# Kernel optimization log

Measured on AMD Instinct MI355X. Metric: run time of the kernel, lower is better.

Reference implementation:

```python
import jax, jax.numpy as jnp
import numpy as np

NUM_HEADS = 12

def setup_inputs() -> dict:
    key = jax.random.key(0)
    k1, k2, k3 = jax.random.split(key, 3)
    B, N, D = 16, 1024, 768
    x = jax.random.normal(k1, (B, N, D), dtype=jnp.float32)
    w_qkv = jax.random.normal(k2, (D, 3 * D), dtype=jnp.float32) * (D ** -0.5)
    b_qkv = jnp.zeros((3 * D,), dtype=jnp.float32)
    w_proj = jax.random.normal(k3, (D, D), dtype=jnp.float32) * (D ** -0.5)
    b_proj = jnp.zeros((D,), dtype=jnp.float32)
    return {"x": x, "w_qkv": w_qkv, "b_qkv": b_qkv, "w_proj": w_proj, "b_proj": b_proj}

def reference(x, w_qkv, b_qkv, w_proj, b_proj):
    B, N, D = x.shape
    H = NUM_HEADS
    Hd = D // H
    scale = Hd ** -0.5
    qkv = x @ w_qkv + b_qkv                       # (B, N, 3D)
    qkv = qkv.reshape(B, N, 3, H, Hd)
    q, k, v = qkv[:, :, 0], qkv[:, :, 1], qkv[:, :, 2]  # (B, N, H, Hd)
    attn = jnp.einsum('bnhd,bmhd->bhnm', q, k) * scale  # (B, H, N, N)
    attn = jax.nn.softmax(attn, axis=-1)
    out = jnp.einsum('bhnm,bmhd->bnhd', attn, v).reshape(B, N, D)
    return out @ w_proj + b_proj
```

## Files before the change

kernel.cpp:

```cpp
#include <hip/hip_runtime.h>


typedef _Float16 half8 __attribute__((ext_vector_type(8)));
typedef _Float16 half4 __attribute__((ext_vector_type(4)));
typedef __fp16   fp16x2 __attribute__((ext_vector_type(2)));
typedef float    f32x4  __attribute__((ext_vector_type(4)));
typedef float    f32x16 __attribute__((ext_vector_type(16)));
typedef unsigned int u32x4 __attribute__((ext_vector_type(4)));

#define DI __device__ __forceinline__

constexpr int   BATCH  = 16;
constexpr int   SEQ    = 1024;
constexpr int   DM     = 768;
constexpr int   NH     = 12;
constexpr int   HD     = 64;
constexpr float SCALE  = 0.125f;
constexpr float LOG2E  = 1.4426950408889634f;

DI void async16(const _Float16* g, _Float16* l) {
  __builtin_amdgcn_global_load_lds(
      (const __attribute__((address_space(1))) void*)g,
      (__attribute__((address_space(3))) void*)l, 16, 0, 0);
}

DI void copy16(_Float16* dst, const _Float16* src) {
  *(u32x4*)dst = *(const u32x4*)src;
}

DI int pack_rtz(float a, float b) {
  union { fp16x2 h; int i; } u;
  u.h = __builtin_amdgcn_cvt_pkrtz(a, b);
  return u.i;
}

__global__ void cvt_x_kernel(const float* __restrict__ x,
                             _Float16* __restrict__ xh, int n4) {
  int i = blockIdx.x * 256 + threadIdx.x;
  if (i >= n4) return;
  float4 v = ((const float4*)x)[i];
  half4 h;
  h[0] = (_Float16)v.x; h[1] = (_Float16)v.y;
  h[2] = (_Float16)v.z; h[3] = (_Float16)v.w;
  *(half4*)(xh + (size_t)i * 4) = h;
}

__global__ void cvt_wt_kernel(const float* __restrict__ w,
                              _Float16* __restrict__ wt, int K, int N) {
  __shared__ float tile[32][33];
  int kb = blockIdx.x * 32, nb = blockIdx.y * 32;
  int tx = threadIdx.x & 31, ty = threadIdx.x >> 5;
#pragma unroll
  for (int i = 0; i < 32; i += 8)
    tile[ty + i][tx] = w[(size_t)(kb + ty + i) * N + nb + tx];
  __syncthreads();
#pragma unroll
  for (int i = 0; i < 32; i += 8)
    wt[(size_t)(nb + ty + i) * K + kb + tx] = (_Float16)tile[tx][ty + i];
}

__launch_bounds__(256)
__global__ void gemm_qkv_kernel(const _Float16* __restrict__ A,
                                const _Float16* __restrict__ Bt,
                                const float* __restrict__ bias,
                                _Float16* __restrict__ Qo,
                                _Float16* __restrict__ Ko,
                                _Float16* __restrict__ VTo) {
  __shared__ _Float16 As[128 * 32];
  __shared__ _Float16 Bs[128 * 32];
  __shared__ _Float16 Cs[128 * 136];
  const int tid  = threadIdx.x;
  const int ct   = blockIdx.x;
  const int m0   = blockIdx.y * 128;
  const int n0   = ct * 128;
  const int w    = tid >> 6, lane = tid & 63;
  const int quad = lane >> 4, l15 = lane & 15;
  const int wr   = w >> 1, wc = w & 1;

  f32x4 acc[4][4] = {};

  const int e  = tid * 8;
  const int rA = e >> 5;
  const int kA = e & 31;
  const _Float16* ga = A  + (size_t)(m0 + rA) * 768 + kA;
  const _Float16* gb = Bt + (size_t)(n0 + rA) * 768 + kA;

  for (int kt = 0; kt < 24; ++kt) {
    __syncthreads();
    const int k0 = kt * 32;
    async16(ga + k0,            &As[e]);
    async16(ga + k0 + 64 * 768, &As[e + 2048]);
    async16(gb + k0,            &Bs[e]);
    async16(gb + k0 + 64 * 768, &Bs[e + 2048]);
    __syncthreads();

    half8 af[4], bf[4];
#pragma unroll
    for (int mi = 0; mi < 4; mi++)
      af[mi] = *(const half8*)&As[(wr * 64 + mi * 16 + l15) * 32 + quad * 8];
#pragma unroll
    for (int ni = 0; ni < 4; ni++)
      bf[ni] = *(const half8*)&Bs[(wc * 64 + ni * 16 + l15) * 32 + quad * 8];
#pragma unroll
    for (int mi = 0; mi < 4; mi++)
#pragma unroll
      for (int ni = 0; ni < 4; ni++)
        acc[mi][ni] = __builtin_amdgcn_mfma_f32_16x16x32_f16(
            af[mi], bf[ni], acc[mi][ni], 0, 0, 0);
  }

  const float oscale = (ct < 6) ? SCALE : 1.0f;
  float bcol[4];
#pragma unroll
  for (int ni = 0; ni < 4; ni++)
    bcol[ni] = bias[n0 + wc * 64 + ni * 16 + l15];
#pragma unroll
  for (int mi = 0; mi < 4; mi++)
#pragma unroll
    for (int ni = 0; ni < 4; ni++) {
      int col = wc * 64 + ni * 16 + l15;
      int row = wr * 64 + mi * 16 + quad * 4;
#pragma unroll
      for (int r = 0; r < 4; r++)
        Cs[(row + r) * 136 + col] = (_Float16)((acc[mi][ni][r] + bcol[ni]) * oscale);
    }
  __syncthreads();

  const int b     = m0 >> 10;
  const int nrow0 = m0 & 1023;
  const int sec   = ct / 6;
  const int h0    = (ct % 6) * 2;

  if (sec < 2) {
    _Float16* dst = (sec == 0) ? Qo : Ko;
    int r = tid >> 1, hl = tid & 1;
    _Float16* g = dst + ((size_t)((b * NH + h0 + hl) * SEQ + nrow0 + r)) * HD;
    const _Float16* s = &Cs[r * 136 + hl * 64];
#pragma unroll
    for (int j = 0; j < 8; j++) copy16(g + j * 8, s + j * 8);
  } else {
    int c = tid >> 1, hf = tid & 1;
    int hl = c >> 6, d = c & 63;
    _Float16 tmp[64];
#pragma unroll
    for (int j = 0; j < 64; j++) tmp[j] = Cs[(hf * 64 + j) * 136 + c];
    _Float16* g = VTo + ((size_t)((b * NH + h0 + hl) * HD + d)) * SEQ
                      + nrow0 + hf * 64;
#pragma unroll
    for (int j = 0; j < 8; j++) copy16(g + j * 8, (const _Float16*)&tmp[j * 8]);
  }
}

__launch_bounds__(256, 2)
__global__ void attn_kernel(const _Float16* __restrict__ Q,
                            const _Float16* __restrict__ K,
                            const _Float16* __restrict__ VT,
                            _Float16* __restrict__ Oh) {
  __shared__ _Float16 smem[2][2][64 * 72];
  _Float16* OLds = &smem[0][0][0];

  const int tid = threadIdx.x;
  const int i   = blockIdx.x;
  const int bh  = (i & 7) * 24 + ((i >> 3) >> 2);
  const int q0  = ((i >> 3) & 3) * 256;
  const int b   = bh / NH, hh = bh - b * NH;
  const int w   = tid >> 6, lane = tid & 63;
  const int l31 = lane & 31, h = lane >> 5;

  const _Float16* Qg = Q  + (size_t)bh * SEQ * HD;
  const _Float16* Kg = K  + (size_t)bh * SEQ * HD;
  const _Float16* Vg = VT + (size_t)bh * HD * SEQ;

  half8 qb[2][4];
#pragma unroll
  for (int N = 0; N < 2; N++) {
    const _Float16* qrow = Qg + (size_t)(q0 + w * 64 + N * 32 + l31) * HD + h * 8;
#pragma unroll
    for (int s = 0; s < 4; s++)
      qb[N][s] = *(const half8*)(qrow + s * 16);
  }

  const int  sr  = (tid & 127) >> 1;
  const int  sp  = tid & 1;
  const bool isK = tid < 128;
  const _Float16* sg = isK ? (Kg + sr * HD + sp * 32)
                           : (Vg + (size_t)sr * SEQ + sp * 32);
  const int sstep = isK ? 64 * HD : 64;
  const int soff  = (isK ? 0 : 64 * 72) + sr * 72 + sp * 32;

  u32x4 pf[4];
#pragma unroll
  for (int c = 0; c < 4; c++) pf[c] = *(const u32x4*)(sg + c * 8);
#pragma unroll
  for (int c = 0; c < 4; c++) *(u32x4*)(&smem[0][0][0] + soff + c * 8) = pf[c];

  f32x16 of[2][2];
#pragma unroll
  for (int D = 0; D < 2; D++)
#pragma unroll
    for (int N = 0; N < 2; N++)
#pragma unroll
      for (int r = 0; r < 16; r++) of[D][N][r] = 0.f;
  float m_[2] = {-1e30f, -1e30f}, l_[2] = {0.f, 0.f};

  for (int kt = 0; kt < 16; ++kt) {
    if (kt < 15) {
      const _Float16* nsg = sg + (kt + 1) * sstep;
#pragma unroll
      for (int c = 0; c < 4; c++) pf[c] = *(const u32x4*)(nsg + c * 8);
    }
    __syncthreads();
    const _Float16* Ks = &smem[kt & 1][0][0];
    const _Float16* Vs = &smem[kt & 1][1][0];

    f32x16 sf[2][2];
#pragma unroll
    for (int M = 0; M < 2; M++)
#pragma unroll
      for (int N = 0; N < 2; N++)
#pragma unroll
        for (int r = 0; r < 16; r++) sf[M][N][r] = 0.f;
#pragma unroll
    for (int s = 0; s < 4; s++) {
      half8 ka0 = *(const half8*)&Ks[l31 * 72 + s * 16 + h * 8];
      half8 ka1 = *(const half8*)&Ks[(32 + l31) * 72 + s * 16 + h * 8];
#pragma unroll
      for (int N = 0; N < 2; N++) {
        sf[0][N] = __builtin_amdgcn_mfma_f32_32x32x16_f16(ka0, qb[N][s], sf[0][N], 0, 0, 0);
        sf[1][N] = __builtin_amdgcn_mfma_f32_32x32x16_f16(ka1, qb[N][s], sf[1][N], 0, 0, 0);
      }
    }

    float alpha[2], c1[2], tsum[2];
#pragma unroll
    for (int N = 0; N < 2; N++) {
      float tmax = -1e30f;
#pragma unroll
      for (int r = 0; r < 16; r++)
        tmax = fmaxf(tmax, fmaxf(sf[0][N][r], sf[1][N][r]));
      tmax = fmaxf(tmax, __shfl_xor(tmax, 32, 64));
      float mnew = fmaxf(m_[N], tmax);
      alpha[N] = __builtin_amdgcn_exp2f((m_[N] - mnew) * LOG2E);
      m_[N] = mnew;
      c1[N] = mnew * LOG2E;
      tsum[N] = 0.f;
    }

    int pdw[2][2][8];
#pragma unroll
    for (int M = 0; M < 2; M++)
#pragma unroll
      for (int N = 0; N < 2; N++) {
#pragma unroll
        for (int r = 0; r < 16; r++) {
          float p = __builtin_amdgcn_exp2f(sf[M][N][r] * LOG2E - c1[N]);
          sf[M][N][r] = p;
          tsum[N] += p;
        }
#pragma unroll
        for (int u = 0; u < 8; u++)
          pdw[M][N][u] = pack_rtz(sf[M][N][2 * u], sf[M][N][2 * u + 1]);
      }
#pragma unroll
    for (int N = 0; N < 2; N++) {
      tsum[N] += __shfl_xor(tsum[N], 32, 64);
      l_[N] = l_[N] * alpha[N] + tsum[N];
    }
#pragma unroll
    for (int D = 0; D < 2; D++)
#pragma unroll
      for (int N = 0; N < 2; N++)
#pragma unroll
        for (int r = 0; r < 16; r++) of[D][N][r] *= alpha[N];

#pragma unroll
    for (int t = 0; t < 4; ++t) {
      const int M = t >> 1, s2 = (t & 1) * 4;
      half8 va0 = *(const half8*)&Vs[l31 * 72 + t * 16 + h * 8];
      half8 va1 = *(const half8*)&Vs[(32 + l31) * 72 + t * 16 + h * 8];
#pragma unroll
      for (int N = 0; N < 2; N++) {
        int a0 = pdw[M][N][s2 + 0], a1 = pdw[M][N][s2 + 1];
        int a2 = pdw[M][N][s2 + 2], a3 = pdw[M][N][s2 + 3];
        int e0 = h ? a0 : a2, e1 = h ? a1 : a3;
        int r0 = __shfl_xor(e0, 32, 64), r1 = __shfl_xor(e1, 32, 64);
        union { u32x4 u; half8 hv; } bb;
        bb.u[0] = h ? r0 : a0; bb.u[1] = h ? r1 : a1;
        bb.u[2] = h ? a2 : r0; bb.u[3] = h ? a3 : r1;
        of[0][N] = __builtin_amdgcn_mfma_f32_32x32x16_f16(va0, bb.hv, of[0][N], 0, 0, 0);
        of[1][N] = __builtin_amdgcn_mfma_f32_32x32x16_f16(va1, bb.hv, of[1][N], 0, 0, 0);
      }
    }

    if (kt < 15) {
      _Float16* dst = &smem[(kt + 1) & 1][0][0] + soff;
#pragma unroll
      for (int c = 0; c < 4; c++) *(u32x4*)(dst + c * 8) = pf[c];
    }
  }

  __syncthreads();
  float inv[2] = {1.0f / l_[0], 1.0f / l_[1]};
  int* OW = (int*)OLds;
#pragma unroll
  for (int N = 0; N < 2; N++) {
    const int q_local = w * 64 + N * 32 + l31;
#pragma unroll
    for (int D = 0; D < 2; D++)
#pragma unroll
      for (int u = 0; u < 8; u++) {
        int v = pack_rtz(of[D][N][2 * u] * inv[N], of[D][N][2 * u + 1] * inv[N]);
        int dwi = 16 * D + 4 * (u >> 1) + (u & 1) + 2 * h;
        OW[q_local * 36 + dwi] = v;
      }
  }
  __syncthreads();
#pragma unroll
  for (int p = 0; p < 8; p++) {
    int q = p * 32 + (tid >> 3), c = tid & 7;
    *(u32x4*)(Oh + (size_t)(b * SEQ + q0 + q) * DM + hh * HD + c * 8) =
        *(const u32x4*)&OLds[q * 72 + c * 8];
  }
}

__launch_bounds__(256)
__global__ void gemm_proj_kernel(const _Float16* __restrict__ A,
                                 const _Float16* __restrict__ Bt,
                                 const float* __restrict__ bias,
                                 float* __restrict__ out) {
  __shared__ _Float16 As[128 * 32];
  __shared__ _Float16 Bs[128 * 32];
  const int tid  = threadIdx.x;
  const int m0   = blockIdx.y * 128;
  const int n0   = blockIdx.x * 128;
  const int w    = tid >> 6, lane = tid & 63;
  const int quad = lane >> 4, l15 = lane & 15;
  const int wr   = w >> 1, wc = w & 1;

  f32x4 acc[4][4] = {};

  const int e  = tid * 8;
  const int rA = e >> 5;
  const int kA = e & 31;
  const _Float16* ga = A  + (size_t)(m0 + rA) * 768 + kA;
  const _Float16* gb = Bt + (size_t)(n0 + rA) * 768 + kA;

  for (int kt = 0; kt < 24; ++kt) {
    __syncthreads();
    const int k0 = kt * 32;
    async16(ga + k0,            &As[e]);
    async16(ga + k0 + 64 * 768, &As[e + 2048]);
    async16(gb + k0,            &Bs[e]);
    async16(gb + k0 + 64 * 768, &Bs[e + 2048]);
    __syncthreads();

    half8 af[4], bf[4];
#pragma unroll
    for (int mi = 0; mi < 4; mi++)
      af[mi] = *(const half8*)&As[(wr * 64 + mi * 16 + l15) * 32 + quad * 8];
#pragma unroll
    for (int ni = 0; ni < 4; ni++)
      bf[ni] = *(const half8*)&Bs[(wc * 64 + ni * 16 + l15) * 32 + quad * 8];
#pragma unroll
    for (int mi = 0; mi < 4; mi++)
#pragma unroll
      for (int ni = 0; ni < 4; ni++)
        acc[mi][ni] = __builtin_amdgcn_mfma_f32_16x16x32_f16(
            af[mi], bf[ni], acc[mi][ni], 0, 0, 0);
  }

  float bcol[4];
#pragma unroll
  for (int ni = 0; ni < 4; ni++)
    bcol[ni] = bias[n0 + wc * 64 + ni * 16 + l15];
#pragma unroll
  for (int mi = 0; mi < 4; mi++)
#pragma unroll
    for (int ni = 0; ni < 4; ni++) {
      int col = n0 + wc * 64 + ni * 16 + l15;
      int row = m0 + wr * 64 + mi * 16 + quad * 4;
#pragma unroll
      for (int r = 0; r < 4; r++)
        out[(size_t)(row + r) * 768 + col] = acc[mi][ni][r] + bcol[ni];
    }
}

extern "C" void kernel_launch(void* const* d_in, const int* in_sizes, int n_in,
                              void* d_out, int out_size, void* d_ws, size_t ws_size,
                              hipStream_t stream) {
  const float* x      = (const float*)d_in[0];
  const float* w_qkv  = (const float*)d_in[1];
  const float* b_qkv  = (const float*)d_in[2];
  const float* w_proj = (const float*)d_in[3];
  const float* b_proj = (const float*)d_in[4];
  float* out = (float*)d_out;

  char* ws = (char*)d_ws;
  _Float16* xh     = (_Float16*)(ws);
  _Float16* wqkvT  = (_Float16*)(ws + 25165824);
  _Float16* wprojT = (_Float16*)(ws + 28704768);
  _Float16* Qp     = (_Float16*)(ws + 29884416);
  _Float16* Kp     = (_Float16*)(ws + 55050240);
  _Float16* VTp    = (_Float16*)(ws + 80216064);
  _Float16* Ohp    = (_Float16*)(ws + 105381888);

  cvt_x_kernel<<<dim3(3145728 / 256), 256, 0, stream>>>(x, xh, 3145728);
  cvt_wt_kernel<<<dim3(24, 72), 256, 0, stream>>>(w_qkv, wqkvT, 768, 2304);
  cvt_wt_kernel<<<dim3(24, 24), 256, 0, stream>>>(w_proj, wprojT, 768, 768);
  gemm_qkv_kernel<<<dim3(18, 128), 256, 0, stream>>>(xh, wqkvT, b_qkv, Qp, Kp, VTp);
  attn_kernel<<<dim3(768), 256, 0, stream>>>(Qp, Kp, VTp, Ohp);
  gemm_proj_kernel<<<dim3(6, 128), 256, 0, stream>>>(Ohp, wprojT, b_proj, out);
}
```

Measured before the change: 321.2 us.

## Merge weight conversions, remap GEMM blocks per XCD, halve epilogue LDS

Merges the two weight-transpose conversion kernels into a single launch. Both GEMMs now use a 1-D grid remapped so that consecutive blocks on the same XCD share A rows, aiming for better L2 reuse. The QKV GEMM epilogue now stages its output tile through LDS in two 64-row halves, shrinking Cs so that with launch_bounds(256,4) more blocks fit per CU. The two-pass epilogue adds an extra barrier, and the occupancy hint may force register limits.

```diff
diff --git a/kernel.cpp b/kernel.cpp
--- a/kernel.cpp
+++ b/kernel.cpp
@@ -45,10 +45,17 @@
   *(half4*)(xh + (size_t)i * 4) = h;
 }
 
-__global__ void cvt_wt_kernel(const float* __restrict__ w,
-                              _Float16* __restrict__ wt, int K, int N) {
+__global__ void cvt_wt2_kernel(const float* __restrict__ wq,
+                               _Float16* __restrict__ wqT,
+                               const float* __restrict__ wp,
+                               _Float16* __restrict__ wpT) {
   __shared__ float tile[32][33];
-  int kb = blockIdx.x * 32, nb = blockIdx.y * 32;
+  const int by = blockIdx.y;
+  const float* w; _Float16* wt; int N, nb;
+  if (by < 72) { w = wq; wt = wqT; N = 2304; nb = by * 32; }
+  else         { w = wp; wt = wpT; N = 768;  nb = (by - 72) * 32; }
+  const int K = 768;
+  int kb = blockIdx.x * 32;
   int tx = threadIdx.x & 31, ty = threadIdx.x >> 5;
 #pragma unroll
   for (int i = 0; i < 32; i += 8)
@@ -59,7 +66,7 @@
     wt[(size_t)(nb + ty + i) * K + kb + tx] = (_Float16)tile[tx][ty + i];
 }
 
-__launch_bounds__(256)
+__launch_bounds__(256, 4)
 __global__ void gemm_qkv_kernel(const _Float16* __restrict__ A,
                                 const _Float16* __restrict__ Bt,
                                 const float* __restrict__ bias,
@@ -68,10 +75,12 @@
                                 _Float16* __restrict__ VTo) {
   __shared__ _Float16 As[128 * 32];
   __shared__ _Float16 Bs[128 * 32];
-  __shared__ _Float16 Cs[128 * 136];
+  __shared__ _Float16 Cs[64 * 136];
   const int tid  = threadIdx.x;
-  const int ct   = blockIdx.x;
-  const int m0   = blockIdx.y * 128;
+  const int lin  = blockIdx.x;
+  const int xcd  = lin & 7, j = lin >> 3;
+  const int ct   = j % 18;
+  const int m0   = ((j / 18) * 8 + xcd) * 128;
   const int n0   = ct * 128;
   const int w    = tid >> 6, lane = tid & 63;
   const int quad = lane >> 4, l15 = lane & 15;
@@ -114,40 +123,53 @@
 #pragma unroll
   for (int ni = 0; ni < 4; ni++)
     bcol[ni] = bias[n0 + wc * 64 + ni * 16 + l15];
-#pragma unroll
-  for (int mi = 0; mi < 4; mi++)
-#pragma unroll
-    for (int ni = 0; ni < 4; ni++) {
-      int col = wc * 64 + ni * 16 + l15;
-      int row = wr * 64 + mi * 16 + quad * 4;
-#pragma unroll
-      for (int r = 0; r < 4; r++)
-        Cs[(row + r) * 136 + col] = (_Float16)((acc[mi][ni][r] + bcol[ni]) * oscale);
-    }
-  __syncthreads();
 
   const int b     = m0 >> 10;
   const int nrow0 = m0 & 1023;
   const int sec   = ct / 6;
   const int h0    = (ct % 6) * 2;
 
-  if (sec < 2) {
-    _Float16* dst = (sec == 0) ? Qo : Ko;
-    int r = tid >> 1, hl = tid & 1;
-    _Float16* g = dst + ((size_t)((b * NH + h0 + hl) * SEQ + nrow0 + r)) * HD;
-    const _Float16* s = &Cs[r * 136 + hl * 64];
-#pragma unroll
-    for (int j = 0; j < 8; j++) copy16(g + j * 8, s + j * 8);
-  } else {
-    int c = tid >> 1, hf = tid & 1;
-    int hl = c >> 6, d = c & 63;
-    _Float16 tmp[64];
-#pragma unroll
-    for (int j = 0; j < 64; j++) tmp[j] = Cs[(hf * 64 + j) * 136 + c];
-    _Float16* g = VTo + ((size_t)((b * NH + h0 + hl) * HD + d)) * SEQ
-                      + nrow0 + hf * 64;
-#pragma unroll
-    for (int j = 0; j < 8; j++) copy16(g + j * 8, (const _Float16*)&tmp[j * 8]);
+#pragma unroll
+  for (int p = 0; p < 2; ++p) {
+    if (p) __syncthreads();
+    if (wr == p) {
+#pragma unroll
+      for (int mi = 0; mi < 4; mi++)
+#pragma unroll
+        for (int ni = 0; ni < 4; ni++) {
+          int col = wc * 64 + ni * 16 + l15;
+          int row = mi * 16 + quad * 4;
+#pragma unroll
+          for (int r = 0; r < 4; r++)
+            Cs[(row + r) * 136 + col] =
+                (_Float16)((acc[mi][ni][r] + bcol[ni]) * oscale);
+        }
+    }
+    __syncthreads();
+
+    if (sec < 2) {
+      _Float16* dst = (sec == 0) ? Qo : Ko;
+      int row = tid >> 2, seg = tid & 3;
+      int hl = seg >> 1, off32 = (seg & 1) * 32;
+      _Float16* g = dst +
+          ((size_t)((b * NH + h0 + hl) * SEQ + nrow0 + p * 64 + row)) * HD + off32;
+      const _Float16* s = &Cs[row * 136 + hl * 64 + off32];
+      copy16(g, s);
+      copy16(g + 8, s + 8);
+      copy16(g + 16, s + 16);
+      copy16(g + 24, s + 24);
+    } else {
+      int c = tid & 127, half = tid >> 7;
+      int hl = c >> 6, d = c & 63;
+      _Float16 tmp[32];
+#pragma unroll
+      for (int jj = 0; jj < 32; jj++) tmp[jj] = Cs[(half * 32 + jj) * 136 + c];
+      _Float16* g = VTo + ((size_t)((b * NH + h0 + hl) * HD + d)) * SEQ
+                        + nrow0 + p * 64 + half * 32;
+#pragma unroll
+      for (int jj = 0; jj < 4; jj++)
+        copy16(g + jj * 8, (const _Float16*)&tmp[jj * 8]);
+    }
   }
 }
 
@@ -323,7 +345,7 @@
   }
 }
 
-__launch_bounds__(256)
+__launch_bounds__(256, 4)
 __global__ void gemm_proj_kernel(const _Float16* __restrict__ A,
                                  const _Float16* __restrict__ Bt,
                                  const float* __restrict__ bias,
@@ -331,8 +353,11 @@
   __shared__ _Float16 As[128 * 32];
   __shared__ _Float16 Bs[128 * 32];
   const int tid  = threadIdx.x;
-  const int m0   = blockIdx.y * 128;
-  const int n0   = blockIdx.x * 128;
+  const int lin  = blockIdx.x;
+  const int xcd  = lin & 7, j = lin >> 3;
+  const int ct   = j % 6;
+  const int m0   = ((j / 6) * 8 + xcd) * 128;
+  const int n0   = ct * 128;
   const int w    = tid >> 6, lane = tid & 63;
   const int quad = lane >> 4, l15 = lane & 15;
   const int wr   = w >> 1, wc = w & 1;
@@ -405,9 +430,8 @@
   _Float16* Ohp    = (_Float16*)(ws + 105381888);
 
   cvt_x_kernel<<<dim3(3145728 / 256), 256, 0, stream>>>(x, xh, 3145728);
-  cvt_wt_kernel<<<dim3(24, 72), 256, 0, stream>>>(w_qkv, wqkvT, 768, 2304);
-  cvt_wt_kernel<<<dim3(24, 24), 256, 0, stream>>>(w_proj, wprojT, 768, 768);
-  gemm_qkv_kernel<<<dim3(18, 128), 256, 0, stream>>>(xh, wqkvT, b_qkv, Qp, Kp, VTp);
+  cvt_wt2_kernel<<<dim3(24, 96), 256, 0, stream>>>(w_qkv, wqkvT, w_proj, wprojT);
+  gemm_qkv_kernel<<<dim3(2304), 256, 0, stream>>>(xh, wqkvT, b_qkv, Qp, Kp, VTp);
   attn_kernel<<<dim3(768), 256, 0, stream>>>(Qp, Kp, VTp, Ohp);
-  gemm_proj_kernel<<<dim3(6, 128), 256, 0, stream>>>(Ohp, wprojT, b_proj, out);
-}
+  gemm_proj_kernel<<<dim3(768), 256, 0, stream>>>(Ohp, wprojT, b_proj, out);
+}
```

Result: faster. 310.6 us (-3.3%).
